# Kernel optimization log

Hardware: AMD Instinct MI355X
Metric: run time of the kernel (lower is better)

The kernel has to match this reference:

```python
import jax, jax.numpy as jnp
import numpy as np
from jax import lax

K = 3
PAD = 1
STRIDE = 1


def setup_inputs() -> dict:
    key = jax.random.key(0)
    k1, k2, k3 = jax.random.split(key, 3)
    B, Cin, Cout, H, W = 4, 64, 64, 128, 128
    x = jax.random.normal(k1, (B, Cin, H, W), dtype=jnp.float32)
    # offset-generating conv weight: [2*K*K, Cin, K, K]
    w_offset = jax.random.normal(k2, (2 * K * K, Cin, K, K), dtype=jnp.float32) * 0.05
    # deformable conv weight: [Cout, Cin, K, K]
    w_deform = jax.random.normal(k3, (Cout, Cin, K, K), dtype=jnp.float32) * 0.05
    return {"x": x, "w_offset": w_offset, "w_deform": w_deform}


def _bilinear_sample_one(img, ys, xs):
    # img: [C, H, W]; ys, xs: [K2, Ho, Wo] float sampling coords
    H, W = img.shape[1], img.shape[2]
    y0 = jnp.floor(ys)
    x0 = jnp.floor(xs)
    wy = ys - y0  # frac weights, [K2, Ho, Wo]
    wx = xs - x0

    def gather(yi, xi):
        valid = (yi >= 0) & (yi <= H - 1) & (xi >= 0) & (xi <= W - 1)
        yc = jnp.clip(yi, 0, H - 1).astype(jnp.int32)
        xc = jnp.clip(xi, 0, W - 1).astype(jnp.int32)
        # img[:, yc, xc] -> [C, K2, Ho, Wo]; zero outside (torchvision zero-pad)
        return img[:, yc, xc] * valid[None].astype(img.dtype)

    v00 = gather(y0, x0)
    v01 = gather(y0, x0 + 1)
    v10 = gather(y0 + 1, x0)
    v11 = gather(y0 + 1, x0 + 1)
    w00 = ((1 - wy) * (1 - wx))[None]
    w01 = ((1 - wy) * wx)[None]
    w10 = (wy * (1 - wx))[None]
    w11 = (wy * wx)[None]
    return v00 * w00 + v01 * w01 + v10 * w10 + v11 * w11  # [C, K2, Ho, Wo]


def reference(x, w_offset, w_deform):
    B, Cin, H, W = x.shape
    Cout = w_deform.shape[0]
    K2 = K * K
    # 1) plain conv to produce offsets: [B, 2*K2, H, W]
    offset = lax.conv_general_dilated(
        x, w_offset, window_strides=(STRIDE, STRIDE),
        padding=((PAD, PAD), (PAD, PAD)),
        dimension_numbers=("NCHW", "OIHW", "NCHW"))
    Ho, Wo = offset.shape[2], offset.shape[3]
    # torchvision ordering: channel 2*k = dy, 2*k+1 = dx, taps row-major
    off = offset.reshape(B, K2, 2, Ho, Wo)
    dy, dx = off[:, :, 0], off[:, :, 1]  # [B, K2, Ho, Wo]
    # 2) base sampling grid per kernel tap
    kk = jnp.arange(K2)
    ki = (kk // K).astype(jnp.float32)  # tap row
    kj = (kk % K).astype(jnp.float32)   # tap col
    base_y = (jnp.arange(Ho, dtype=jnp.float32) * STRIDE - PAD)[None, :] + ki[:, None]  # [K2, Ho]
    base_x = (jnp.arange(Wo, dtype=jnp.float32) * STRIDE - PAD)[None, :] + kj[:, None]  # [K2, Wo]
    ys = base_y[None, :, :, None] + dy  # [B, K2, Ho, Wo]
    xs = base_x[None, :, None, :] + dx
    # 3) deformable bilinear gather: [B, Cin, K2, Ho, Wo]
    sampled = jax.vmap(_bilinear_sample_one)(x, ys, xs)
    # 4) weighted accumulation (the conv contraction)
    out = jnp.einsum("ock,bckhw->bohw", w_deform.reshape(Cout, Cin, K2), sampled)
    return out
```

## Files before the change

### kernel.cpp

```cpp
#include <hip/hip_runtime.h>


#define BATCH 4
#define CIN   64
#define COUT  64
#define HH    128
#define WW    128
#define HWPIX (HH*WW)

typedef __attribute__((ext_vector_type(8))) short short8;
typedef __attribute__((ext_vector_type(4))) float floatx4;

__device__ __forceinline__ unsigned short f2bf(float f) {
  unsigned int u = __float_as_uint(f);
  unsigned int r = u + 0x7fffu + ((u >> 16) & 1u);
  return (unsigned short)(r >> 16);
}
__device__ __forceinline__ float bf2f(unsigned short h) { return __uint_as_float(((unsigned int)h) << 16); }
__device__ __forceinline__ float lo16f(unsigned int u) { return __uint_as_float(u << 16); }
__device__ __forceinline__ float hi16f(unsigned int u) { return __uint_as_float(u & 0xffff0000u); }

__device__ __forceinline__ unsigned int bilin2(unsigned int u00, unsigned int u01,
                                               unsigned int u10, unsigned int u11,
                                               float w00, float w01, float w10, float w11) {
  float lo = w00 * lo16f(u00) + w01 * lo16f(u01) + w10 * lo16f(u10) + w11 * lo16f(u11);
  float hi = w00 * hi16f(u00) + w01 * hi16f(u01) + w10 * hi16f(u10) + w11 * hi16f(u11);
  unsigned int r;
  asm("v_cvt_pk_bf16_f32 %0, %1, %2" : "=v"(r) : "v"(lo), "v"(hi));
  return r;
}

__device__ __forceinline__ int swz(int a) { return a ^ (((a >> 9) & 3) << 4); }

__global__ __launch_bounds__(256) void pre_kernel(const float* __restrict__ x,
                                                  const float* __restrict__ wo,
                                                  const float* __restrict__ wd,
                                                  unsigned short* __restrict__ xThi,
                                                  unsigned short* __restrict__ xTlo,
                                                  unsigned short* __restrict__ wdA,
                                                  unsigned short* __restrict__ woAhi,
                                                  unsigned short* __restrict__ woAlo) {
  int tid = threadIdx.x;
  if (blockIdx.x < 4096) {
    __shared__ float tile[32][33];
    int t = blockIdx.x;
    int b = t >> 10, rem = t & 1023;
    int c0 = (rem >> 9) * 32, p0 = (rem & 511) * 32;
    int tx = tid & 31, ty = tid >> 5;
    const float* xb = x + (size_t)b * CIN * HWPIX;
    size_t boff = (size_t)b * HWPIX * CIN;
#pragma unroll
    for (int i = 0; i < 4; i++)
      tile[ty + i * 8][tx] = xb[(size_t)(c0 + ty + i * 8) * HWPIX + p0 + tx];
    __syncthreads();
#pragma unroll
    for (int i = 0; i < 2; i++) {
      int tt = tid + i * 256;
      int row = tt >> 4;
      int cp = tt & 15;
      float v0 = tile[cp * 2][row], v1 = tile[cp * 2 + 1][row];
      unsigned short h0 = f2bf(v0), h1 = f2bf(v1);
      unsigned short l0 = f2bf(v0 - bf2f(h0)), l1 = f2bf(v1 - bf2f(h1));
      size_t o = boff + (size_t)(p0 + row) * CIN + c0 + cp * 2;
      *(ushort2*)&xThi[o] = make_ushort2(h0, h1);
      *(ushort2*)&xTlo[o] = make_ushort2(l0, l1);
    }
  } else {
    int t = (blockIdx.x - 4096) * 256 + tid;
    if (t < 36864) {
      int j = t & 7, lane = (t >> 3) & 63, ct = (t >> 9) & 3, kc = (t >> 11) & 1, kk = t >> 12;
      int cout = ct * 16 + (lane & 15);
      int cin  = kc * 32 + (lane >> 4) * 8 + j;
      wdA[t] = f2bf(wd[(size_t)(cout * CIN + cin) * 9 + kk]);
    }
    int t2 = t - 36864;
    if (t2 >= 0 && t2 < 18432) {
      int j = t2 & 7, lane = (t2 >> 3) & 63, ct = (t2 >> 9) & 1, kc = (t2 >> 10) & 1, kk = t2 >> 11;
      int cout = ct * 16 + (lane & 15);
      int cin  = kc * 32 + (lane >> 4) * 8 + j;
      float v = (cout < 18) ? wo[(size_t)(cout * CIN + cin) * 9 + kk] : 0.f;
      unsigned short h = f2bf(v);
      woAhi[t2] = h;
      woAlo[t2] = f2bf(v - bf2f(h));
    }
  }
}

__global__ __launch_bounds__(256) void fused_dcn_kernel(const unsigned short* __restrict__ xThi,
                                                        const unsigned short* __restrict__ xTlo,
                                                        const unsigned short* __restrict__ woAhi,
                                                        const unsigned short* __restrict__ woAlo,
                                                        const unsigned short* __restrict__ wdA,
                                                        float* __restrict__ out) {
  __shared__ unsigned short sBhi2[2][4096];
  __shared__ unsigned short sBlo2[2][4096];
  __shared__ float offL[18 * 64];
  char* sHc = (char*)sBhi2;
  char* sLc = (char*)sBlo2;

  int tid = threadIdx.x;
  int hw = blockIdx.x;
  int bid = (hw & 7) * 128 + (hw >> 3);
  int b = bid >> 8, r = bid & 255, y = r >> 1, x0 = (r & 1) << 6;

  int p1 = tid >> 2, si = tid & 3;
  int lane = tid & 63, w = tid >> 6;

  const unsigned short* xhib = xThi + (size_t)b * HWPIX * CIN;
  const unsigned short* xlob = xTlo + (size_t)b * HWPIX * CIN;

  int wq = p1 >> 4, iq = p1 & 15;
  int kcd = si >> 1, qb = si & 1;
  int wb0 = ((((wq * 2 + kcd) * 64) + qb * 32 + iq) * 8) * 2;
  int wb1 = wb0 + 256;
  int swb0 = swz(wb0), swb1 = swz(wb1);
  int brb0[4], brb1[4];
#pragma unroll
  for (int pg = 0; pg < 4; pg++) {
    brb0[pg] = swz(pg * 2048 + lane * 16);
    brb1[pg] = swz(pg * 2048 + 1024 + lane * 16);
  }

  int xp = x0 + p1;

  floatx4 oacc[2];
  oacc[0] = (floatx4){0.f, 0.f, 0.f, 0.f};
  oacc[1] = (floatx4){0.f, 0.f, 0.f, 0.f};
  int ctA = w & 1, pgA = (w >> 1) * 2;

  auto ldA = [&](int kk, uint4& h0, uint4& h1, uint4& l0, uint4& l1) {
    int ys = y - 1 + kk / 3;
    int xs = xp - 1 + kk % 3;
    bool valid = (ys >= 0) && (ys < HH) && (xs >= 0) && (xs < WW);
    h0 = (uint4){0, 0, 0, 0}; h1 = h0; l0 = h0; l1 = h0;
    if (valid) {
      const unsigned short* ph = xhib + (size_t)(ys * WW + xs) * CIN + si * 16;
      const unsigned short* pl = xlob + (size_t)(ys * WW + xs) * CIN + si * 16;
      h0 = *(const uint4*)ph; h1 = *(const uint4*)(ph + 8);
      l0 = *(const uint4*)pl; l1 = *(const uint4*)(pl + 8);
    }
  };
  auto stageA = [&](int nxt, const uint4& h0, const uint4& h1, const uint4& l0, const uint4& l1) {
    *(uint4*)(sHc + nxt * 8192 + swb0) = h0;
    *(uint4*)(sHc + nxt * 8192 + swb1) = h1;
    *(uint4*)(sLc + nxt * 8192 + swb0) = l0;
    *(uint4*)(sLc + nxt * 8192 + swb1) = l1;
  };
  auto mfmaA = [&](int kk, int cur) {
    const short8* Ah = (const short8*)(woAhi + (size_t)kk * 2048);
    const short8* Al = (const short8*)(woAlo + (size_t)kk * 2048);
    short8 ah0 = Ah[ctA * 64 + lane], ah1 = Ah[128 + ctA * 64 + lane];
    short8 al0 = Al[ctA * 64 + lane], al1 = Al[128 + ctA * 64 + lane];
#pragma unroll
    for (int pgi = 0; pgi < 2; pgi++) {
      int pg = pgA + pgi;
      short8 bh0 = *(const short8*)(sHc + cur * 8192 + brb0[pg]);
      short8 bh1 = *(const short8*)(sHc + cur * 8192 + brb1[pg]);
      short8 bl0 = *(const short8*)(sLc + cur * 8192 + brb0[pg]);
      short8 bl1 = *(const short8*)(sLc + cur * 8192 + brb1[pg]);
      oacc[pgi] = __builtin_amdgcn_mfma_f32_16x16x32_bf16(ah0, bh0, oacc[pgi], 0, 0, 0);
      oacc[pgi] = __builtin_amdgcn_mfma_f32_16x16x32_bf16(ah0, bl0, oacc[pgi], 0, 0, 0);
      oacc[pgi] = __builtin_amdgcn_mfma_f32_16x16x32_bf16(al0, bh0, oacc[pgi], 0, 0, 0);
      oacc[pgi] = __builtin_amdgcn_mfma_f32_16x16x32_bf16(ah1, bh1, oacc[pgi], 0, 0, 0);
      oacc[pgi] = __builtin_amdgcn_mfma_f32_16x16x32_bf16(ah1, bl1, oacc[pgi], 0, 0, 0);
      oacc[pgi] = __builtin_amdgcn_mfma_f32_16x16x32_bf16(al1, bh1, oacc[pgi], 0, 0, 0);
    }
  };

  {
    uint4 h0c, h1c, l0c, l1c;
    ldA(0, h0c, h1c, l0c, l1c);
    stageA(0, h0c, h1c, l0c, l1c);
    __syncthreads();
#pragma unroll 1
    for (int kk = 0; kk < 9; kk++) {
      uint4 h0n, h1n, l0n, l1n;
      if (kk < 8) ldA(kk + 1, h0n, h1n, l0n, l1n);
      mfmaA(kk, kk & 1);
      if (kk < 8) stageA((kk + 1) & 1, h0n, h1n, l0n, l1n);
      __syncthreads();
    }
  }

  {
    int rowb = (lane >> 4) * 4;
    int colb = pgA * 16 + (lane & 15);
#pragma unroll
    for (int pgi = 0; pgi < 2; pgi++)
#pragma unroll
      for (int rr = 0; rr < 4; rr++) {
        int row = ctA * 16 + rowb + rr;
        if (row < 18) offL[row * 64 + colb + pgi * 16] = oacc[pgi][rr];
      }
  }
  __syncthreads();

  floatx4 acc[4];
#pragma unroll
  for (int pg = 0; pg < 4; pg++) acc[pg] = (floatx4){0.f, 0.f, 0.f, 0.f};

  struct BS {
    float w00, w01, w10, w11;
    uint4 a00, a01, a10, a11, b00, b01, b10, b11;
  };
  auto ldB = [&](int kk) -> BS {
    BS s;
    float dy = offL[(2 * kk) * 64 + p1];
    float dx = offL[(2 * kk + 1) * 64 + p1];
    float ys = (float)(y - 1 + kk / 3) + dy;
    float xs = (float)(xp - 1 + kk % 3) + dx;
    float y0f = floorf(ys), x0f = floorf(xs);
    float wy = ys - y0f, wx = xs - x0f;
    int iy0 = (int)y0f, ix0 = (int)x0f;
    int iy1 = iy0 + 1, ix1 = ix0 + 1;
    s.w00 = (1.f - wy) * (1.f - wx); s.w01 = (1.f - wy) * wx;
    s.w10 = wy * (1.f - wx);         s.w11 = wy * wx;
    bool vy0 = (iy0 >= 0) && (iy0 < HH), vy1 = (iy1 >= 0) && (iy1 < HH);
    bool vx0 = (ix0 >= 0) && (ix0 < WW), vx1 = (ix1 >= 0) && (ix1 < WW);
    if (!(vy0 && vx0)) s.w00 = 0.f;
    if (!(vy0 && vx1)) s.w01 = 0.f;
    if (!(vy1 && vx0)) s.w10 = 0.f;
    if (!(vy1 && vx1)) s.w11 = 0.f;
    int cy0 = min(max(iy0, 0), HH - 1), cy1 = min(max(iy1, 0), HH - 1);
    int cx0 = min(max(ix0, 0), WW - 1), cx1 = min(max(ix1, 0), WW - 1);
    const unsigned short* q00 = xhib + (size_t)(cy0 * WW + cx0) * CIN + si * 16;
    const unsigned short* q01 = xhib + (size_t)(cy0 * WW + cx1) * CIN + si * 16;
    const unsigned short* q10 = xhib + (size_t)(cy1 * WW + cx0) * CIN + si * 16;
    const unsigned short* q11 = xhib + (size_t)(cy1 * WW + cx1) * CIN + si * 16;
    s.a00 = *(const uint4*)q00; s.a01 = *(const uint4*)q01;
    s.a10 = *(const uint4*)q10; s.a11 = *(const uint4*)q11;
    s.b00 = *(const uint4*)(q00 + 8); s.b01 = *(const uint4*)(q01 + 8);
    s.b10 = *(const uint4*)(q10 + 8); s.b11 = *(const uint4*)(q11 + 8);
    return s;
  };
  auto blendStoreB = [&](int nxt, const BS& s) {
    uint4 o0, o1;
    o0.x = bilin2(s.a00.x, s.a01.x, s.a10.x, s.a11.x, s.w00, s.w01, s.w10, s.w11);
    o0.y = bilin2(s.a00.y, s.a01.y, s.a10.y, s.a11.y, s.w00, s.w01, s.w10, s.w11);
    o0.z = bilin2(s.a00.z, s.a01.z, s.a10.z, s.a11.z, s.w00, s.w01, s.w10, s.w11);
    o0.w = bilin2(s.a00.w, s.a01.w, s.a10.w, s.a11.w, s.w00, s.w01, s.w10, s.w11);
    o1.x = bilin2(s.b00.x, s.b01.x, s.b10.x, s.b11.x, s.w00, s.w01, s.w10, s.w11);
    o1.y = bilin2(s.b00.y, s.b01.y, s.b10.y, s.b11.y, s.w00, s.w01, s.w10, s.w11);
    o1.z = bilin2(s.b00.z, s.b01.z, s.b10.z, s.b11.z, s.w00, s.w01, s.w10, s.w11);
    o1.w = bilin2(s.b00.w, s.b01.w, s.b10.w, s.b11.w, s.w00, s.w01, s.w10, s.w11);
    *(uint4*)(sHc + nxt * 8192 + swb0) = o0;
    *(uint4*)(sHc + nxt * 8192 + swb1) = o1;
  };
  auto mfmaB = [&](int kk, int cur) {
    const short8* Ap = (const short8*)(wdA + (size_t)kk * 4096);
    short8 a0 = Ap[w * 64 + lane];
    short8 a1 = Ap[256 + w * 64 + lane];
#pragma unroll
    for (int pg = 0; pg < 4; pg++) {
      short8 bv0 = *(const short8*)(sHc + cur * 8192 + brb0[pg]);
      short8 bv1 = *(const short8*)(sHc + cur * 8192 + brb1[pg]);
      acc[pg] = __builtin_amdgcn_mfma_f32_16x16x32_bf16(a0, bv0, acc[pg], 0, 0, 0);
      acc[pg] = __builtin_amdgcn_mfma_f32_16x16x32_bf16(a1, bv1, acc[pg], 0, 0, 0);
    }
  };

  {
    BS s0 = ldB(0);
    blendStoreB(0, s0);
    __syncthreads();
#pragma unroll 1
    for (int kk = 0; kk < 9; kk++) {
      BS sn;
      if (kk < 8) sn = ldB(kk + 1);
      mfmaB(kk, kk & 1);
      if (kk < 8) blendStoreB((kk + 1) & 1, sn);
      __syncthreads();
    }
  }

  int rowb = (lane >> 4) * 4;
  float* outb = out + (size_t)b * COUT * HWPIX + y * WW + x0 + (lane & 15);
#pragma unroll
  for (int pg = 0; pg < 4; pg++)
#pragma unroll
    for (int rr = 0; rr < 4; rr++)
      outb[(size_t)(w * 16 + rowb + rr) * HWPIX + pg * 16] = acc[pg][rr];
}

extern "C" void kernel_launch(void* const* d_in, const int* in_sizes, int n_in,
                              void* d_out, int out_size, void* d_ws, size_t ws_size,
                              hipStream_t stream) {
  const float* x  = (const float*)d_in[0];
  const float* wo = (const float*)d_in[1];
  const float* wd = (const float*)d_in[2];
  float* out = (float*)d_out;

  char* wsb = (char*)d_ws;
  unsigned short* xThi  = (unsigned short*)wsb;
  unsigned short* xTlo  = (unsigned short*)(wsb + 8388608);
  unsigned short* wdA   = (unsigned short*)(wsb + 16777216);
  unsigned short* woAhi = (unsigned short*)(wsb + 16777216 + 73728);
  unsigned short* woAlo = (unsigned short*)(wsb + 16850944 + 36864);

  pre_kernel<<<dim3(4096 + 216), dim3(256), 0, stream>>>(x, wo, wd, xThi, xTlo, wdA, woAhi, woAlo);
  fused_dcn_kernel<<<dim3(BATCH * HWPIX / 64), dim3(256), 0, stream>>>(xThi, xTlo, woAhi, woAlo, wdA, out);
}
```

Measured before the change: 106.0 us.

## Stage 3x66 halo rows in LDS once for the offset conv

```diff
diff --git a/kernel.cpp b/kernel.cpp
--- a/kernel.cpp
+++ b/kernel.cpp
@@ -7,6 +7,7 @@
 #define HH    128
 #define WW    128
 #define HWPIX (HH*WW)
+#define ROWS_LO 25344
 
 typedef __attribute__((ext_vector_type(8))) short short8;
 typedef __attribute__((ext_vector_type(4))) float floatx4;
@@ -31,6 +32,7 @@
 }
 
 __device__ __forceinline__ int swz(int a) { return a ^ (((a >> 9) & 3) << 4); }
+__device__ __forceinline__ int swzR(int a) { return a ^ (((a >> 7) & 7) << 4); }
 
 __global__ __launch_bounds__(256) void pre_kernel(const float* __restrict__ x,
                                                   const float* __restrict__ wo,
@@ -92,11 +94,8 @@
                                                         const unsigned short* __restrict__ woAlo,
                                                         const unsigned short* __restrict__ wdA,
                                                         float* __restrict__ out) {
-  __shared__ unsigned short sBhi2[2][4096];
-  __shared__ unsigned short sBlo2[2][4096];
-  __shared__ float offL[18 * 64];
-  char* sHc = (char*)sBhi2;
-  char* sLc = (char*)sBlo2;
+  __shared__ char pool[50688];
+  float* offL = (float*)(pool + 16384);
 
   int tid = threadIdx.x;
   int hw = blockIdx.x;
@@ -105,10 +104,73 @@
 
   int p1 = tid >> 2, si = tid & 3;
   int lane = tid & 63, w = tid >> 6;
+  int colp = lane & 15, g = lane >> 4;
 
   const unsigned short* xhib = xThi + (size_t)b * HWPIX * CIN;
   const unsigned short* xlob = xTlo + (size_t)b * HWPIX * CIN;
 
+  for (int t = tid; t < 1584; t += 256) {
+    int ri = t / 528;
+    int rem = t - ri * 528;
+    int xi = rem >> 3, sl = rem & 7;
+    int ys = y - 1 + ri, xs = x0 - 1 + xi;
+    uint4 vh = {0, 0, 0, 0}, vl = {0, 0, 0, 0};
+    if (ys >= 0 && ys < HH && xs >= 0 && xs < WW) {
+      const unsigned short* ph = xhib + (size_t)(ys * WW + xs) * CIN + sl * 8;
+      const unsigned short* pl = xlob + (size_t)(ys * WW + xs) * CIN + sl * 8;
+      vh = *(const uint4*)ph; vl = *(const uint4*)pl;
+    }
+    int a = t * 16;
+    *(uint4*)(pool + swzR(a)) = vh;
+    *(uint4*)(pool + ROWS_LO + swzR(a)) = vl;
+  }
+  __syncthreads();
+
+  floatx4 oacc[2];
+  oacc[0] = (floatx4){0.f, 0.f, 0.f, 0.f};
+  oacc[1] = (floatx4){0.f, 0.f, 0.f, 0.f};
+  int ctA = w & 1, pgA = (w >> 1) * 2;
+
+#pragma unroll
+  for (int kk = 0; kk < 9; kk++) {
+    int kd = kk / 3, km = kk % 3;
+    const short8* Ah = (const short8*)(woAhi + (size_t)kk * 2048);
+    const short8* Al = (const short8*)(woAlo + (size_t)kk * 2048);
+    short8 ah0 = Ah[ctA * 64 + lane], ah1 = Ah[128 + ctA * 64 + lane];
+    short8 al0 = Al[ctA * 64 + lane], al1 = Al[128 + ctA * 64 + lane];
+#pragma unroll
+    for (int pgi = 0; pgi < 2; pgi++) {
+      int xi = (pgA + pgi) * 16 + colp + km;
+      int ab = (kd * 66 + xi) * 128 + g * 16;
+      short8 bh0 = *(const short8*)(pool + swzR(ab));
+      short8 bh1 = *(const short8*)(pool + swzR(ab + 64));
+      short8 bl0 = *(const short8*)(pool + ROWS_LO + swzR(ab));
+      short8 bl1 = *(const short8*)(pool + ROWS_LO + swzR(ab + 64));
+      oacc[pgi] = __builtin_amdgcn_mfma_f32_16x16x32_bf16(ah0, bh0, oacc[pgi], 0, 0, 0);
+      oacc[pgi] = __builtin_amdgcn_mfma_f32_16x16x32_bf16(ah0, bl0, oacc[pgi], 0, 0, 0);
+      oacc[pgi] = __builtin_amdgcn_mfma_f32_16x16x32_bf16(al0, bh0, oacc[pgi], 0, 0, 0);
+      oacc[pgi] = __builtin_amdgcn_mfma_f32_16x16x32_bf16(ah1, bh1, oacc[pgi], 0, 0, 0);
+      oacc[pgi] = __builtin_amdgcn_mfma_f32_16x16x32_bf16(ah1, bl1, oacc[pgi], 0, 0, 0);
+      oacc[pgi] = __builtin_amdgcn_mfma_f32_16x16x32_bf16(al1, bh1, oacc[pgi], 0, 0, 0);
+    }
+  }
+
+  __syncthreads();
+
+  {
+    int rowb = (lane >> 4) * 4;
+    int colb = pgA * 16 + colp;
+#pragma unroll
+    for (int pgi = 0; pgi < 2; pgi++)
+#pragma unroll
+      for (int rr = 0; rr < 4; rr++) {
+        int row = ctA * 16 + rowb + rr;
+        if (row < 18) offL[row * 64 + colb + pgi * 16] = oacc[pgi][rr];
+      }
+  }
+  __syncthreads();
+
+  char* sHc = pool;
   int wq = p1 >> 4, iq = p1 & 15;
   int kcd = si >> 1, qb = si & 1;
   int wb0 = ((((wq * 2 + kcd) * 64) + qb * 32 + iq) * 8) * 2;
@@ -120,80 +182,7 @@
     brb0[pg] = swz(pg * 2048 + lane * 16);
     brb1[pg] = swz(pg * 2048 + 1024 + lane * 16);
   }
-
   int xp = x0 + p1;
-
-  floatx4 oacc[2];
-  oacc[0] = (floatx4){0.f, 0.f, 0.f, 0.f};
-  oacc[1] = (floatx4){0.f, 0.f, 0.f, 0.f};
-  int ctA = w & 1, pgA = (w >> 1) * 2;
-
-  auto ldA = [&](int kk, uint4& h0, uint4& h1, uint4& l0, uint4& l1) {
-    int ys = y - 1 + kk / 3;
-    int xs = xp - 1 + kk % 3;
-    bool valid = (ys >= 0) && (ys < HH) && (xs >= 0) && (xs < WW);
-    h0 = (uint4){0, 0, 0, 0}; h1 = h0; l0 = h0; l1 = h0;
-    if (valid) {
-      const unsigned short* ph = xhib + (size_t)(ys * WW + xs) * CIN + si * 16;
-      const unsigned short* pl = xlob + (size_t)(ys * WW + xs) * CIN + si * 16;
-      h0 = *(const uint4*)ph; h1 = *(const uint4*)(ph + 8);
-      l0 = *(const uint4*)pl; l1 = *(const uint4*)(pl + 8);
-    }
-  };
-  auto stageA = [&](int nxt, const uint4& h0, const uint4& h1, const uint4& l0, const uint4& l1) {
-    *(uint4*)(sHc + nxt * 8192 + swb0) = h0;
-    *(uint4*)(sHc + nxt * 8192 + swb1) = h1;
-    *(uint4*)(sLc + nxt * 8192 + swb0) = l0;
-    *(uint4*)(sLc + nxt * 8192 + swb1) = l1;
-  };
-  auto mfmaA = [&](int kk, int cur) {
-    const short8* Ah = (const short8*)(woAhi + (size_t)kk * 2048);
-    const short8* Al = (const short8*)(woAlo + (size_t)kk * 2048);
-    short8 ah0 = Ah[ctA * 64 + lane], ah1 = Ah[128 + ctA * 64 + lane];
-    short8 al0 = Al[ctA * 64 + lane], al1 = Al[128 + ctA * 64 + lane];
-#pragma unroll
-    for (int pgi = 0; pgi < 2; pgi++) {
-      int pg = pgA + pgi;
-      short8 bh0 = *(const short8*)(sHc + cur * 8192 + brb0[pg]);
-      short8 bh1 = *(const short8*)(sHc + cur * 8192 + brb1[pg]);
-      short8 bl0 = *(const short8*)(sLc + cur * 8192 + brb0[pg]);
-      short8 bl1 = *(const short8*)(sLc + cur * 8192 + brb1[pg]);
-      oacc[pgi] = __builtin_amdgcn_mfma_f32_16x16x32_bf16(ah0, bh0, oacc[pgi], 0, 0, 0);
-      oacc[pgi] = __builtin_amdgcn_mfma_f32_16x16x32_bf16(ah0, bl0, oacc[pgi], 0, 0, 0);
-      oacc[pgi] = __builtin_amdgcn_mfma_f32_16x16x32_bf16(al0, bh0, oacc[pgi], 0, 0, 0);
-      oacc[pgi] = __builtin_amdgcn_mfma_f32_16x16x32_bf16(ah1, bh1, oacc[pgi], 0, 0, 0);
-      oacc[pgi] = __builtin_amdgcn_mfma_f32_16x16x32_bf16(ah1, bl1, oacc[pgi], 0, 0, 0);
-      oacc[pgi] = __builtin_amdgcn_mfma_f32_16x16x32_bf16(al1, bh1, oacc[pgi], 0, 0, 0);
-    }
-  };
-
-  {
-    uint4 h0c, h1c, l0c, l1c;
-    ldA(0, h0c, h1c, l0c, l1c);
-    stageA(0, h0c, h1c, l0c, l1c);
-    __syncthreads();
-#pragma unroll 1
-    for (int kk = 0; kk < 9; kk++) {
-      uint4 h0n, h1n, l0n, l1n;
-      if (kk < 8) ldA(kk + 1, h0n, h1n, l0n, l1n);
-      mfmaA(kk, kk & 1);
-      if (kk < 8) stageA((kk + 1) & 1, h0n, h1n, l0n, l1n);
-      __syncthreads();
-    }
-  }
-
-  {
-    int rowb = (lane >> 4) * 4;
-    int colb = pgA * 16 + (lane & 15);
-#pragma unroll
-    for (int pgi = 0; pgi < 2; pgi++)
-#pragma unroll
-      for (int rr = 0; rr < 4; rr++) {
-        int row = ctA * 16 + rowb + rr;
-        if (row < 18) offL[row * 64 + colb + pgi * 16] = oacc[pgi][rr];
-      }
-  }
-  __syncthreads();
 
   floatx4 acc[4];
 #pragma unroll
@@ -274,7 +263,7 @@
   }
 
   int rowb = (lane >> 4) * 4;
-  float* outb = out + (size_t)b * COUT * HWPIX + y * WW + x0 + (lane & 15);
+  float* outb = out + (size_t)b * COUT * HWPIX + y * WW + x0 + colp;
 #pragma unroll
   for (int pg = 0; pg < 4; pg++)
 #pragma unroll
```

Result: slower. 110.8 us (+4.6%).

## Halve pixel tile to 32 per block, doubling block count and thread-per-channel split

Applied to the files above, without the earlier changes.

```diff
diff --git a/kernel.cpp b/kernel.cpp
--- a/kernel.cpp
+++ b/kernel.cpp
@@ -30,7 +30,7 @@
   return r;
 }
 
-__device__ __forceinline__ int swz(int a) { return a ^ (((a >> 9) & 3) << 4); }
+__device__ __forceinline__ int swzB(int a) { return a ^ (((a >> 8) & 7) << 4); }
 
 __global__ __launch_bounds__(256) void pre_kernel(const float* __restrict__ x,
                                                   const float* __restrict__ wo,
@@ -92,121 +92,106 @@
                                                         const unsigned short* __restrict__ woAlo,
                                                         const unsigned short* __restrict__ wdA,
                                                         float* __restrict__ out) {
-  __shared__ unsigned short sBhi2[2][4096];
-  __shared__ unsigned short sBlo2[2][4096];
-  __shared__ float offL[18 * 64];
+  __shared__ unsigned short sBhi2[2][2048];
+  __shared__ unsigned short sBlo2[2][2048];
+  __shared__ float offL[18 * 32];
   char* sHc = (char*)sBhi2;
   char* sLc = (char*)sBlo2;
 
   int tid = threadIdx.x;
   int hw = blockIdx.x;
-  int bid = (hw & 7) * 128 + (hw >> 3);
-  int b = bid >> 8, r = bid & 255, y = r >> 1, x0 = (r & 1) << 6;
-
-  int p1 = tid >> 2, si = tid & 3;
+  int bid = (hw & 7) * 256 + (hw >> 3);
+  int b = bid >> 9, r = bid & 511, y = r >> 2, x0 = (r & 3) << 5;
+
+  int p1 = tid >> 3, o = tid & 7;
   int lane = tid & 63, w = tid >> 6;
+  int colp = lane & 15;
 
   const unsigned short* xhib = xThi + (size_t)b * HWPIX * CIN;
   const unsigned short* xlob = xTlo + (size_t)b * HWPIX * CIN;
 
-  int wq = p1 >> 4, iq = p1 & 15;
-  int kcd = si >> 1, qb = si & 1;
-  int wb0 = ((((wq * 2 + kcd) * 64) + qb * 32 + iq) * 8) * 2;
-  int wb1 = wb0 + 256;
-  int swb0 = swz(wb0), swb1 = swz(wb1);
-  int brb0[4], brb1[4];
-#pragma unroll
-  for (int pg = 0; pg < 4; pg++) {
-    brb0[pg] = swz(pg * 2048 + lane * 16);
-    brb1[pg] = swz(pg * 2048 + 1024 + lane * 16);
-  }
+  int pgS = p1 >> 4, iq = p1 & 15, kcS = o >> 2, gS = o & 3;
+  int sab = swzB(pgS * 2048 + kcS * 1024 + gS * 256 + iq * 16);
+  int rAB[2][2];
+#pragma unroll
+  for (int pg = 0; pg < 2; pg++)
+#pragma unroll
+    for (int kc = 0; kc < 2; kc++)
+      rAB[pg][kc] = swzB(pg * 2048 + kc * 1024 + lane * 16);
 
   int xp = x0 + p1;
 
-  floatx4 oacc[2];
-  oacc[0] = (floatx4){0.f, 0.f, 0.f, 0.f};
-  oacc[1] = (floatx4){0.f, 0.f, 0.f, 0.f};
-  int ctA = w & 1, pgA = (w >> 1) * 2;
-
-  auto ldA = [&](int kk, uint4& h0, uint4& h1, uint4& l0, uint4& l1) {
+  floatx4 oaccA = (floatx4){0.f, 0.f, 0.f, 0.f};
+  int ctA = w & 1, pgW = w >> 1;
+
+  auto ldA = [&](int kk, uint4& h, uint4& l) {
     int ys = y - 1 + kk / 3;
     int xs = xp - 1 + kk % 3;
     bool valid = (ys >= 0) && (ys < HH) && (xs >= 0) && (xs < WW);
-    h0 = (uint4){0, 0, 0, 0}; h1 = h0; l0 = h0; l1 = h0;
+    h = (uint4){0, 0, 0, 0}; l = h;
     if (valid) {
-      const unsigned short* ph = xhib + (size_t)(ys * WW + xs) * CIN + si * 16;
-      const unsigned short* pl = xlob + (size_t)(ys * WW + xs) * CIN + si * 16;
-      h0 = *(const uint4*)ph; h1 = *(const uint4*)(ph + 8);
-      l0 = *(const uint4*)pl; l1 = *(const uint4*)(pl + 8);
-    }
-  };
-  auto stageA = [&](int nxt, const uint4& h0, const uint4& h1, const uint4& l0, const uint4& l1) {
-    *(uint4*)(sHc + nxt * 8192 + swb0) = h0;
-    *(uint4*)(sHc + nxt * 8192 + swb1) = h1;
-    *(uint4*)(sLc + nxt * 8192 + swb0) = l0;
-    *(uint4*)(sLc + nxt * 8192 + swb1) = l1;
+      h = *(const uint4*)(xhib + (size_t)(ys * WW + xs) * CIN + o * 8);
+      l = *(const uint4*)(xlob + (size_t)(ys * WW + xs) * CIN + o * 8);
+    }
+  };
+  auto stageA = [&](int nxt, const uint4& h, const uint4& l) {
+    *(uint4*)(sHc + nxt * 4096 + sab) = h;
+    *(uint4*)(sLc + nxt * 4096 + sab) = l;
   };
   auto mfmaA = [&](int kk, int cur) {
     const short8* Ah = (const short8*)(woAhi + (size_t)kk * 2048);
     const short8* Al = (const short8*)(woAlo + (size_t)kk * 2048);
     short8 ah0 = Ah[ctA * 64 + lane], ah1 = Ah[128 + ctA * 64 + lane];
     short8 al0 = Al[ctA * 64 + lane], al1 = Al[128 + ctA * 64 + lane];
-#pragma unroll
-    for (int pgi = 0; pgi < 2; pgi++) {
-      int pg = pgA + pgi;
-      short8 bh0 = *(const short8*)(sHc + cur * 8192 + brb0[pg]);
-      short8 bh1 = *(const short8*)(sHc + cur * 8192 + brb1[pg]);
-      short8 bl0 = *(const short8*)(sLc + cur * 8192 + brb0[pg]);
-      short8 bl1 = *(const short8*)(sLc + cur * 8192 + brb1[pg]);
-      oacc[pgi] = __builtin_amdgcn_mfma_f32_16x16x32_bf16(ah0, bh0, oacc[pgi], 0, 0, 0);
-      oacc[pgi] = __builtin_amdgcn_mfma_f32_16x16x32_bf16(ah0, bl0, oacc[pgi], 0, 0, 0);
-      oacc[pgi] = __builtin_amdgcn_mfma_f32_16x16x32_bf16(al0, bh0, oacc[pgi], 0, 0, 0);
-      oacc[pgi] = __builtin_amdgcn_mfma_f32_16x16x32_bf16(ah1, bh1, oacc[pgi], 0, 0, 0);
-      oacc[pgi] = __builtin_amdgcn_mfma_f32_16x16x32_bf16(ah1, bl1, oacc[pgi], 0, 0, 0);
-      oacc[pgi] = __builtin_amdgcn_mfma_f32_16x16x32_bf16(al1, bh1, oacc[pgi], 0, 0, 0);
-    }
+    short8 bh0 = *(const short8*)(sHc + cur * 4096 + rAB[pgW][0]);
+    short8 bh1 = *(const short8*)(sHc + cur * 4096 + rAB[pgW][1]);
+    short8 bl0 = *(const short8*)(sLc + cur * 4096 + rAB[pgW][0]);
+    short8 bl1 = *(const short8*)(sLc + cur * 4096 + rAB[pgW][1]);
+    oaccA = __builtin_amdgcn_mfma_f32_16x16x32_bf16(ah0, bh0, oaccA, 0, 0, 0);
+    oaccA = __builtin_amdgcn_mfma_f32_16x16x32_bf16(ah0, bl0, oaccA, 0, 0, 0);
+    oaccA = __builtin_amdgcn_mfma_f32_16x16x32_bf16(al0, bh0, oaccA, 0, 0, 0);
+    oaccA = __builtin_amdgcn_mfma_f32_16x16x32_bf16(ah1, bh1, oaccA, 0, 0, 0);
+    oaccA = __builtin_amdgcn_mfma_f32_16x16x32_bf16(ah1, bl1, oaccA, 0, 0, 0);
+    oaccA = __builtin_amdgcn_mfma_f32_16x16x32_bf16(al1, bh1, oaccA, 0, 0, 0);
   };
 
   {
-    uint4 h0c, h1c, l0c, l1c;
-    ldA(0, h0c, h1c, l0c, l1c);
-    stageA(0, h0c, h1c, l0c, l1c);
+    uint4 hc, lc;
+    ldA(0, hc, lc);
+    stageA(0, hc, lc);
     __syncthreads();
 #pragma unroll 1
     for (int kk = 0; kk < 9; kk++) {
-      uint4 h0n, h1n, l0n, l1n;
-      if (kk < 8) ldA(kk + 1, h0n, h1n, l0n, l1n);
+      uint4 hn, ln;
+      if (kk < 8) ldA(kk + 1, hn, ln);
       mfmaA(kk, kk & 1);
-      if (kk < 8) stageA((kk + 1) & 1, h0n, h1n, l0n, l1n);
+      if (kk < 8) stageA((kk + 1) & 1, hn, ln);
       __syncthreads();
     }
   }
 
   {
     int rowb = (lane >> 4) * 4;
-    int colb = pgA * 16 + (lane & 15);
-#pragma unroll
-    for (int pgi = 0; pgi < 2; pgi++)
-#pragma unroll
-      for (int rr = 0; rr < 4; rr++) {
-        int row = ctA * 16 + rowb + rr;
-        if (row < 18) offL[row * 64 + colb + pgi * 16] = oacc[pgi][rr];
-      }
+#pragma unroll
+    for (int rr = 0; rr < 4; rr++) {
+      int row = ctA * 16 + rowb + rr;
+      if (row < 18) offL[row * 32 + pgW * 16 + colp] = oaccA[rr];
+    }
   }
   __syncthreads();
 
-  floatx4 acc[4];
-#pragma unroll
-  for (int pg = 0; pg < 4; pg++) acc[pg] = (floatx4){0.f, 0.f, 0.f, 0.f};
+  floatx4 acc[2];
+  acc[0] = (floatx4){0.f, 0.f, 0.f, 0.f};
+  acc[1] = (floatx4){0.f, 0.f, 0.f, 0.f};
 
   struct BS {
     float w00, w01, w10, w11;
-    uint4 a00, a01, a10, a11, b00, b01, b10, b11;
+    uint4 a00, a01, a10, a11;
   };
   auto ldB = [&](int kk) -> BS {
     BS s;
-    float dy = offL[(2 * kk) * 64 + p1];
-    float dx = offL[(2 * kk + 1) * 64 + p1];
+    float dy = offL[(2 * kk) * 32 + p1];
+    float dx = offL[(2 * kk + 1) * 32 + p1];
     float ys = (float)(y - 1 + kk / 3) + dy;
     float xs = (float)(xp - 1 + kk % 3) + dx;
     float y0f = floorf(ys), x0f = floorf(xs);
@@ -223,37 +208,28 @@
     if (!(vy1 && vx1)) s.w11 = 0.f;
     int cy0 = min(max(iy0, 0), HH - 1), cy1 = min(max(iy1, 0), HH - 1);
     int cx0 = min(max(ix0, 0), WW - 1), cx1 = min(max(ix1, 0), WW - 1);
-    const unsigned short* q00 = xhib + (size_t)(cy0 * WW + cx0) * CIN + si * 16;
-    const unsigned short* q01 = xhib + (size_t)(cy0 * WW + cx1) * CIN + si * 16;
-    const unsigned short* q10 = xhib + (size_t)(cy1 * WW + cx0) * CIN + si * 16;
-    const unsigned short* q11 = xhib + (size_t)(cy1 * WW + cx1) * CIN + si * 16;
-    s.a00 = *(const uint4*)q00; s.a01 = *(const uint4*)q01;
-    s.a10 = *(const uint4*)q10; s.a11 = *(const uint4*)q11;
-    s.b00 = *(const uint4*)(q00 + 8); s.b01 = *(const uint4*)(q01 + 8);
-    s.b10 = *(const uint4*)(q10 + 8); s.b11 = *(const uint4*)(q11 + 8);
+    s.a00 = *(const uint4*)(xhib + (size_t)(cy0 * WW + cx0) * CIN + o * 8);
+    s.a01 = *(const uint4*)(xhib + (size_t)(cy0 * WW + cx1) * CIN + o * 8);
+    s.a10 = *(const uint4*)(xhib + (size_t)(cy1 * WW + cx0) * CIN + o * 8);
+    s.a11 = *(const uint4*)(xhib + (size_t)(cy1 * WW + cx1) * CIN + o * 8);
     return s;
   };
   auto blendStoreB = [&](int nxt, const BS& s) {
-    uint4 o0, o1;
+    uint4 o0;
     o0.x = bilin2(s.a00.x, s.a01.x, s.a10.x, s.a11.x, s.w00, s.w01, s.w10, s.w11);
     o0.y = bilin2(s.a00.y, s.a01.y, s.a10.y, s.a11.y, s.w00, s.w01, s.w10, s.w11);
     o0.z = bilin2(s.a00.z, s.a01.z, s.a10.z, s.a11.z, s.w00, s.w01, s.w10, s.w11);
     o0.w = bilin2(s.a00.w, s.a01.w, s.a10.w, s.a11.w, s.w00, s.w01, s.w10, s.w11);
-    o1.x = bilin2(s.b00.x, s.b01.x, s.b10.x, s.b11.x, s.w00, s.w01, s.w10, s.w11);
-    o1.y = bilin2(s.b00.y, s.b01.y, s.b10.y, s.b11.y, s.w00, s.w01, s.w10, s.w11);
-    o1.z = bilin2(s.b00.z, s.b01.z, s.b10.z, s.b11.z, s.w00, s.w01, s.w10, s.w11);
-    o1.w = bilin2(s.b00.w, s.b01.w, s.b10.w, s.b11.w, s.w00, s.w01, s.w10, s.w11);
-    *(uint4*)(sHc + nxt * 8192 + swb0) = o0;
-    *(uint4*)(sHc + nxt * 8192 + swb1) = o1;
+    *(uint4*)(sHc + nxt * 4096 + sab) = o0;
   };
   auto mfmaB = [&](int kk, int cur) {
     const short8* Ap = (const short8*)(wdA + (size_t)kk * 4096);
     short8 a0 = Ap[w * 64 + lane];
     short8 a1 = Ap[256 + w * 64 + lane];
 #pragma unroll
-    for (int pg = 0; pg < 4; pg++) {
-      short8 bv0 = *(const short8*)(sHc + cur * 8192 + brb0[pg]);
-      short8 bv1 = *(const short8*)(sHc + cur * 8192 + brb1[pg]);
+    for (int pg = 0; pg < 2; pg++) {
+      short8 bv0 = *(const short8*)(sHc + cur * 4096 + rAB[pg][0]);
+      short8 bv1 = *(const short8*)(sHc + cur * 4096 + rAB[pg][1]);
       acc[pg] = __builtin_amdgcn_mfma_f32_16x16x32_bf16(a0, bv0, acc[pg], 0, 0, 0);
       acc[pg] = __builtin_amdgcn_mfma_f32_16x16x32_bf16(a1, bv1, acc[pg], 0, 0, 0);
     }
@@ -274,9 +250,9 @@
   }
 
   int rowb = (lane >> 4) * 4;
-  float* outb = out + (size_t)b * COUT * HWPIX + y * WW + x0 + (lane & 15);
-#pragma unroll
-  for (int pg = 0; pg < 4; pg++)
+  float* outb = out + (size_t)b * COUT * HWPIX + y * WW + x0 + colp;
+#pragma unroll
+  for (int pg = 0; pg < 2; pg++)
 #pragma unroll
     for (int rr = 0; rr < 4; rr++)
       outb[(size_t)(w * 16 + rowb + rr) * HWPIX + pg * 16] = acc[pg][rr];
@@ -298,5 +274,5 @@
   unsigned short* woAlo = (unsigned short*)(wsb + 16850944 + 36864);
 
   pre_kernel<<<dim3(4096 + 216), dim3(256), 0, stream>>>(x, wo, wd, xThi, xTlo, wdA, woAhi, woAlo);
-  fused_dcn_kernel<<<dim3(BATCH * HWPIX / 64), dim3(256), 0, stream>>>(xThi, xTlo, woAhi, woAlo, wdA, out);
-}
+  fused_dcn_kernel<<<dim3(2048), dim3(256), 0, stream>>>(xThi, xTlo, woAhi, woAlo, wdA, out);
+}
```

Measured after the change: 109.6 us. 3.4% more time.

## Split fused deformable conv kernel into offset-conv and deformable-gather kernels

Applied to the files above, without the earlier changes.

```diff
diff --git a/kernel.cpp b/kernel.cpp
--- a/kernel.cpp
+++ b/kernel.cpp
@@ -86,15 +86,13 @@
   }
 }
 
-__global__ __launch_bounds__(256) void fused_dcn_kernel(const unsigned short* __restrict__ xThi,
-                                                        const unsigned short* __restrict__ xTlo,
-                                                        const unsigned short* __restrict__ woAhi,
-                                                        const unsigned short* __restrict__ woAlo,
-                                                        const unsigned short* __restrict__ wdA,
-                                                        float* __restrict__ out) {
+__global__ __launch_bounds__(256) void offA_kernel(const unsigned short* __restrict__ xThi,
+                                                   const unsigned short* __restrict__ xTlo,
+                                                   const unsigned short* __restrict__ woAhi,
+                                                   const unsigned short* __restrict__ woAlo,
+                                                   float* __restrict__ offs) {
   __shared__ unsigned short sBhi2[2][4096];
   __shared__ unsigned short sBlo2[2][4096];
-  __shared__ float offL[18 * 64];
   char* sHc = (char*)sBhi2;
   char* sLc = (char*)sBlo2;
 
@@ -184,16 +182,47 @@
 
   {
     int rowb = (lane >> 4) * 4;
-    int colb = pgA * 16 + (lane & 15);
+    float* ob = offs + (size_t)b * 18 * HWPIX + y * WW;
 #pragma unroll
     for (int pgi = 0; pgi < 2; pgi++)
 #pragma unroll
       for (int rr = 0; rr < 4; rr++) {
         int row = ctA * 16 + rowb + rr;
-        if (row < 18) offL[row * 64 + colb + pgi * 16] = oacc[pgi][rr];
+        if (row < 18) ob[(size_t)row * HWPIX + x0 + (pgA + pgi) * 16 + (lane & 15)] = oacc[pgi][rr];
       }
   }
-  __syncthreads();
+}
+
+__global__ __launch_bounds__(256) void defB_kernel(const unsigned short* __restrict__ xThi,
+                                                   const float* __restrict__ offs,
+                                                   const unsigned short* __restrict__ wdA,
+                                                   float* __restrict__ out) {
+  __shared__ unsigned short sB2[2][4096];
+  char* sHc = (char*)sB2;
+
+  int tid = threadIdx.x;
+  int hw = blockIdx.x;
+  int bid = (hw & 7) * 128 + (hw >> 3);
+  int b = bid >> 8, r = bid & 255, y = r >> 1, x0 = (r & 1) << 6;
+
+  int p1 = tid >> 2, si = tid & 3;
+  int lane = tid & 63, w = tid >> 6;
+
+  const unsigned short* xhib = xThi + (size_t)b * HWPIX * CIN;
+  const float* ob = offs + (size_t)b * 18 * HWPIX + y * WW;
+
+  int wq = p1 >> 4, iq = p1 & 15;
+  int kcd = si >> 1, qb = si & 1;
+  int wb0 = ((((wq * 2 + kcd) * 64) + qb * 32 + iq) * 8) * 2;
+  int wb1 = wb0 + 256;
+  int swb0 = swz(wb0), swb1 = swz(wb1);
+  int brb0[4], brb1[4];
+#pragma unroll
+  for (int pg = 0; pg < 4; pg++) {
+    brb0[pg] = swz(pg * 2048 + lane * 16);
+    brb1[pg] = swz(pg * 2048 + 1024 + lane * 16);
+  }
+  int xp = x0 + p1;
 
   floatx4 acc[4];
 #pragma unroll
@@ -205,8 +234,8 @@
   };
   auto ldB = [&](int kk) -> BS {
     BS s;
-    float dy = offL[(2 * kk) * 64 + p1];
-    float dx = offL[(2 * kk + 1) * 64 + p1];
+    float dy = ob[(size_t)(2 * kk) * HWPIX + xp];
+    float dx = ob[(size_t)(2 * kk + 1) * HWPIX + xp];
     float ys = (float)(y - 1 + kk / 3) + dy;
     float xs = (float)(xp - 1 + kk % 3) + dx;
     float y0f = floorf(ys), x0f = floorf(xs);
@@ -293,10 +322,12 @@
   char* wsb = (char*)d_ws;
   unsigned short* xThi  = (unsigned short*)wsb;
   unsigned short* xTlo  = (unsigned short*)(wsb + 8388608);
-  unsigned short* wdA   = (unsigned short*)(wsb + 16777216);
-  unsigned short* woAhi = (unsigned short*)(wsb + 16777216 + 73728);
-  unsigned short* woAlo = (unsigned short*)(wsb + 16850944 + 36864);
+  float* offs           = (float*)(wsb + 16777216);
+  unsigned short* wdA   = (unsigned short*)(wsb + 16777216 + 4718592);
+  unsigned short* woAhi = (unsigned short*)(wsb + 21495808 + 73728);
+  unsigned short* woAlo = (unsigned short*)(wsb + 21569536 + 36864);
 
   pre_kernel<<<dim3(4096 + 216), dim3(256), 0, stream>>>(x, wo, wd, xThi, xTlo, wdA, woAhi, woAlo);
-  fused_dcn_kernel<<<dim3(BATCH * HWPIX / 64), dim3(256), 0, stream>>>(xThi, xTlo, woAhi, woAlo, wdA, out);
-}
+  offA_kernel<<<dim3(BATCH * HWPIX / 64), dim3(256), 0, stream>>>(xThi, xTlo, woAhi, woAlo, offs);
+  defB_kernel<<<dim3(BATCH * HWPIX / 64), dim3(256), 0, stream>>>(xThi, offs, wdA, out);
+}
```

New measurement: 112.6 us. 1.06x slower.
